# Kernel tuning notes

Hardware: AMD Instinct MI355X
Metric: run time of the kernel (lower is better)

The kernel has to match this reference:

```python
import jax, jax.numpy as jnp
import numpy as np

N_NODES = 100000
N_EDGES = 1600000
N_GRAPHS = 256
D = 128      # d_graph
H = 256      # hidden
VOCAB = 30000
OUT = 2


def setup_inputs() -> dict:
    key = jax.random.key(0)
    ks = jax.random.split(key, 24)
    def lin(k, fin, fout):
        s = 1.0 / np.sqrt(fin)
        kw, kb = jax.random.split(k)
        return (jax.random.uniform(kw, (fin, fout), jnp.float32, -s, s),
                jax.random.uniform(kb, (fout,), jnp.float32, -s, s))
    inp = {
        'feat': jax.random.randint(ks[0], (N_NODES,), 0, VOCAB),
        'src': jax.random.randint(ks[1], (N_EDGES,), 0, N_NODES),
        'dst': jax.random.randint(ks[2], (N_EDGES,), 0, N_NODES),
        'graph_id': jnp.sort(jax.random.randint(ks[3], (N_NODES,), 0, N_GRAPHS)),
        'emb': jax.random.normal(ks[4], (VOCAB, D), jnp.float32),
    }
    # SAGEConv layer 0/1: fc_self + fc_neigh + bias (mean aggregator)
    inp['ws0'], _ = lin(ks[5], D, D)
    inp['wn0'], inp['b0'] = lin(ks[6], D, D)
    inp['ws1'], _ = lin(ks[7], D, D)
    inp['wn1'], inp['b1'] = lin(ks[8], D, D)
    inp['e1_w'], inp['e1_b'] = lin(ks[9], D, H)
    inp['e2_w'], inp['e2_b'] = lin(ks[10], H, H)
    inp['e3_w'], inp['e3_b'] = lin(ks[11], H, H)
    inp['e4_w'], inp['e4_b'] = lin(ks[12], H, H)
    inp['pred_w'], inp['pred_b'] = lin(ks[13], H, OUT)
    return inp


def _sage_mean(h, src, dst, ws, wn, b):
    # gather src features, mean-scatter to dst (DGL SAGEConv 'mean')
    msg = jnp.take(h, src, axis=0)                       # [E, D]
    agg = jax.ops.segment_sum(msg, dst, num_segments=N_NODES)
    deg = jax.ops.segment_sum(jnp.ones((src.shape[0],), h.dtype), dst,
                              num_segments=N_NODES)
    h_neigh = agg / jnp.maximum(deg, 1.0)[:, None]
    return h @ ws + h_neigh @ wn + b


def reference(feat, src, dst, graph_id, emb,
              ws0, wn0, b0, ws1, wn1, b1,
              e1_w, e1_b, e2_w, e2_b, e3_w, e3_b, e4_w, e4_b,
              pred_w, pred_b):
    h = jnp.take(emb, feat, axis=0)                      # [N, D]
    h = jax.nn.relu(_sage_mean(h, src, dst, ws0, wn0, b0))
    h = jax.nn.relu(_sage_mean(h, src, dst, ws1, wn1, b1))
    # dgl.mean_nodes: per-graph mean pool
    gsum = jax.ops.segment_sum(h, graph_id, num_segments=N_GRAPHS)
    gcnt = jax.ops.segment_sum(jnp.ones((N_NODES,), h.dtype), graph_id,
                               num_segments=N_GRAPHS)
    hg = gsum / jnp.maximum(gcnt, 1.0)[:, None]          # [B, D]
    hidden = jax.nn.relu(hg @ e1_w + e1_b)
    h2 = jax.nn.relu(hidden @ e2_w + e2_b)
    h3 = jax.nn.relu(h2 @ e3_w + e3_b)
    h4 = jax.nn.relu(h3 @ e4_w + e4_b)
    y = h4 @ pred_w + pred_b
    return jax.nn.log_softmax(y, axis=1), hidden
```

## Files before the change

kernel.cpp:

```cpp
#include <hip/hip_runtime.h>
#include <hip/hip_bf16.h>
#include <math.h>

#define DF 128
#define HID 256
#define NG 256
#define CSR_CAP 768

typedef __attribute__((ext_vector_type(8))) short s8v;
typedef __attribute__((ext_vector_type(4))) float f32x4;
typedef __attribute__((ext_vector_type(2))) float f32x2;

__device__ __forceinline__ unsigned pack2bf(float lo, float hi){
  unsigned a = __bfloat16_as_ushort(__float2bfloat16(lo));
  unsigned b = __bfloat16_as_ushort(__float2bfloat16(hi));
  return a | (b<<16);
}

__global__ __launch_bounds__(256)
void k_pre0(const float* __restrict__ emb, unsigned* __restrict__ emb_f8, int nvoc,
            const int* __restrict__ dst, int* __restrict__ gb,
            const int* __restrict__ gid, float* __restrict__ gcnt,
            const float* __restrict__ ws0, const float* __restrict__ wn0,
            const float* __restrict__ ws1, const float* __restrict__ wn1,
            unsigned short* __restrict__ wt,
            int N, int E, int NC){
  __shared__ int hist[256];
  const int b = blockIdx.x, t = threadIdx.x;
  if (b < NC){
    int idx = b*256 + t;
    int total = nvoc*(DF/8);
    if (idx<total){
      const float4* e4 = (const float4*)emb;
      float4 v0 = e4[(size_t)idx*2], v1 = e4[(size_t)idx*2+1];
      unsigned w0 = __builtin_amdgcn_cvt_pk_fp8_f32(v0.x, v0.y, 0, false);
      w0 = __builtin_amdgcn_cvt_pk_fp8_f32(v0.z, v0.w, w0, true);
      unsigned w1 = __builtin_amdgcn_cvt_pk_fp8_f32(v1.x, v1.y, 0, false);
      w1 = __builtin_amdgcn_cvt_pk_fp8_f32(v1.z, v1.w, w1, true);
      ((uint2*)emb_f8)[idx] = make_uint2(w0,w1);
    }
  } else if (b < NC+256){
    int bb = b - NC;
    hist[t]=0; __syncthreads();
    for (int i = bb*256+t; i < E; i += 256*256)
      atomicAdd(&hist[dst[i]>>9], 1);
    __syncthreads();
    if (hist[t]) atomicAdd(&gb[t], hist[t]);
  } else if (b < NC+512){
    int bb = b - (NC+256);
    hist[t]=0; __syncthreads();
    for (int i = bb*256+t; i < N; i += 256*256)
      atomicAdd(&hist[gid[i]], 1);
    __syncthreads();
    if (hist[t]) atomicAdd(&gcnt[t], (float)hist[t]);
  } else {
    int bb = b - (NC+512);
    int n = bb & 127;
    int layer = bb >> 7;
    const float* ws = layer? ws1 : ws0;
    const float* wn = layer? wn1 : wn0;
    float v = (t<128)? ws[t*DF+n] : wn[(t-128)*DF+n];
    wt[((size_t)layer*DF + n)*256 + t] = __bfloat16_as_ushort(__float2bfloat16(v));
  }
}

__global__ __launch_bounds__(256)
void k_mid(const int* __restrict__ feat, const unsigned* __restrict__ emb_f8,
           unsigned* __restrict__ h_f8, int N,
           const int* __restrict__ src, const int* __restrict__ dst,
           const int* __restrict__ gb, int* __restrict__ bcur,
           unsigned* __restrict__ pairs, int E){
  const int b = blockIdx.x, t = threadIdx.x;
  if (b >= 256){
    int idx = (b-256)*256 + t;
    int total = N*8;
    if (idx<total){
      int i = idx>>3, c = idx&7;
      ((uint4*)h_f8)[idx] = ((const uint4*)emb_f8)[(size_t)feat[i]*8 + c];
    }
    return;
  }
  __shared__ int sgb[256];
  __shared__ int hist[256];
  __shared__ int base[256];
  __shared__ int cur[256];
  const int CH = (E + 255)/256;
  const int s = b*CH;
  int e = s+CH; if (e>E) e=E;
  if (s>=E) return;
  int v = gb[t];
  sgb[t]=v;
  hist[t]=0;
  __syncthreads();
  for (int o=1;o<256;o<<=1){
    int x = (t>=o)? sgb[t-o] : 0;
    __syncthreads();
    sgb[t]+=x;
    __syncthreads();
  }
  int bstart = sgb[t]-v;
  for (int i=s+t; i<e; i+=256) atomicAdd(&hist[dst[i]>>9],1);
  __syncthreads();
  if (hist[t]){ base[t] = bstart + atomicAdd(&bcur[t],hist[t]); }
  cur[t]=0;
  __syncthreads();
  for (int i=s+t; i<e; i+=256){
    int d = dst[i];
    int bk = d>>9;
    int r = atomicAdd(&cur[bk],1);
    pairs[base[bk]+r] = ((unsigned)src[i]<<9) | (unsigned)(d & 511);
  }
}

__global__ __launch_bounds__(256)
void k_bcsr(const unsigned* __restrict__ pairs, const int* __restrict__ gb,
            int* __restrict__ offs, int* __restrict__ csr, int N, int E){
  __shared__ int sgb[256];
  __shared__ int ncnt[512];
  __shared__ int noff[512];
  __shared__ int sh[256];
  const int t = threadIdx.x;
  const int b = blockIdx.x;
  const int nb0 = b<<9;
  int v = gb[t];
  sgb[t]=v;
  ncnt[t]=0; ncnt[t+256]=0;
  __syncthreads();
  for (int o=1;o<256;o<<=1){
    int x = (t>=o)? sgb[t-o] : 0;
    __syncthreads();
    sgb[t]+=x;
    __syncthreads();
  }
  const int s = sgb[b]-gb[b];
  const int e = sgb[b];
  for (int i=s+t; i<e; i+=256) atomicAdd(&ncnt[pairs[i] & 511u], 1);
  __syncthreads();
  int v0 = ncnt[2*t], v1 = ncnt[2*t+1];
  int vv = v0+v1;
  sh[t]=vv; __syncthreads();
  for (int o=1;o<256;o<<=1){
    int x=(t>=o)?sh[t-o]:0;
    __syncthreads();
    sh[t]+=x;
    __syncthreads();
  }
  int ex = sh[t]-vv;
  noff[2*t]=ex; noff[2*t+1]=ex+v0;
  __syncthreads();
  {
    int n0 = nb0 + t;
    if (n0 < N) offs[n0] = s + noff[t];
    int n1 = nb0 + t + 256;
    if (n1 < N) offs[n1] = s + noff[t+256];
    if (b == gridDim.x-1 && t==0) offs[N] = E;
  }
  ncnt[t]=0; ncnt[t+256]=0;
  __syncthreads();
  for (int i=s+t; i<e; i+=256){
    unsigned p = pairs[i];
    int d = p & 511u;
    int r = atomicAdd(&ncnt[d],1);
    csr[s + noff[d] + r] = (int)(p >> 9);
  }
}

template<int MODE>
__global__ __launch_bounds__(256,8)
void k_sage(const unsigned char* __restrict__ h_in_f8,
            const int* __restrict__ offs, const int* __restrict__ csr,
            const unsigned short* __restrict__ wt,
            const float* __restrict__ bias,
            unsigned char* __restrict__ h_out_f8,
            const int* __restrict__ gid, float* __restrict__ gsum, int N){
  __shared__ __align__(16) unsigned short s_ab[32*256];
  __shared__ int s_csr[CSR_CAP];
  __shared__ int s_gid[32];
  __shared__ float s_tmp[DF];
  const int t = threadIdx.x;
  const int node0 = blockIdx.x*32;
  const uint4* f8r = (const uint4*)h_in_f8;

  if (MODE==1 && t<32) s_gid[t] = (node0+t<N)? gid[node0+t] : -1;

  const int eBase = offs[node0];
  const int eTop  = offs[min(node0+32, N)];
  const int ecount = eTop - eBase;
  const bool useLds = (ecount <= CSR_CAP);
  if (useLds){
    for (int i=t; i<ecount; i+=256) s_csr[i] = csr[eBase+i];
  }

  const int nn = t>>3, c = t&7;
  const int sw = (nn&7)<<4;

  {
    int node = node0+nn;
    uint4 q = make_uint4(0,0,0,0);
    if (node<N) q = f8r[(size_t)node*8 + c];
    f32x2 u; unsigned pk[8];
    u=__builtin_amdgcn_cvt_pk_f32_fp8(q.x,false); pk[0]=pack2bf(u[0],u[1]);
    u=__builtin_amdgcn_cvt_pk_f32_fp8(q.x,true ); pk[1]=pack2bf(u[0],u[1]);
    u=__builtin_amdgcn_cvt_pk_f32_fp8(q.y,false); pk[2]=pack2bf(u[0],u[1]);
    u=__builtin_amdgcn_cvt_pk_f32_fp8(q.y,true ); pk[3]=pack2bf(u[0],u[1]);
    u=__builtin_amdgcn_cvt_pk_f32_fp8(q.z,false); pk[4]=pack2bf(u[0],u[1]);
    u=__builtin_amdgcn_cvt_pk_f32_fp8(q.z,true ); pk[5]=pack2bf(u[0],u[1]);
    u=__builtin_amdgcn_cvt_pk_f32_fp8(q.w,false); pk[6]=pack2bf(u[0],u[1]);
    u=__builtin_amdgcn_cvt_pk_f32_fp8(q.w,true ); pk[7]=pack2bf(u[0],u[1]);
    int byte0 = nn*512 + c*32;
    *(uint4*)((char*)s_ab + ((byte0   )^sw)) = make_uint4(pk[0],pk[1],pk[2],pk[3]);
    *(uint4*)((char*)s_ab + ((byte0+16)^sw)) = make_uint4(pk[4],pk[5],pk[6],pk[7]);
  }
  __syncthreads();

  {
    const int node = node0+nn;
    float a[16];
    #pragma unroll
    for (int j=0;j<16;j++) a[j]=0.f;
    if (node<N){
      int e0=offs[node], e1=offs[node+1];
      int deg = e1-e0;
      if (deg>0){
        #define ACC16(q) { \
          f32x2 u; \
          u=__builtin_amdgcn_cvt_pk_f32_fp8((q).x,false); a[0]+=u[0]; a[1]+=u[1]; \
          u=__builtin_amdgcn_cvt_pk_f32_fp8((q).x,true ); a[2]+=u[0]; a[3]+=u[1]; \
          u=__builtin_amdgcn_cvt_pk_f32_fp8((q).y,false); a[4]+=u[0]; a[5]+=u[1]; \
          u=__builtin_amdgcn_cvt_pk_f32_fp8((q).y,true ); a[6]+=u[0]; a[7]+=u[1]; \
          u=__builtin_amdgcn_cvt_pk_f32_fp8((q).z,false); a[8]+=u[0]; a[9]+=u[1]; \
          u=__builtin_amdgcn_cvt_pk_f32_fp8((q).z,true ); a[10]+=u[0]; a[11]+=u[1]; \
          u=__builtin_amdgcn_cvt_pk_f32_fp8((q).w,false); a[12]+=u[0]; a[13]+=u[1]; \
          u=__builtin_amdgcn_cvt_pk_f32_fp8((q).w,true ); a[14]+=u[0]; a[15]+=u[1]; }
        if (useLds){
          int le = e0 - eBase, le1 = e1 - eBase;
          for (; le+2<=le1; le+=2){
            int s0 = s_csr[le], s1 = s_csr[le+1];
            uint4 q0 = f8r[(size_t)s0*8 + c];
            uint4 q1 = f8r[(size_t)s1*8 + c];
            ACC16(q0); ACC16(q1);
          }
          if (le<le1){
            uint4 q0 = f8r[(size_t)s_csr[le]*8 + c];
            ACC16(q0);
          }
        } else {
          int e = e0;
          for (; e+2<=e1; e+=2){
            int s0 = csr[e], s1 = csr[e+1];
            uint4 q0 = f8r[(size_t)s0*8 + c];
            uint4 q1 = f8r[(size_t)s1*8 + c];
            ACC16(q0); ACC16(q1);
          }
          if (e<e1){
            uint4 q0 = f8r[(size_t)csr[e]*8 + c];
            ACC16(q0);
          }
        }
        #undef ACC16
        float inv = 1.0f/(float)deg;
        #pragma unroll
        for (int j=0;j<16;j++) a[j]*=inv;
      }
    }
    unsigned pk[8];
    #pragma unroll
    for (int j=0;j<8;j++) pk[j] = pack2bf(a[2*j],a[2*j+1]);
    int byte0 = nn*512 + 256 + c*32;
    *(uint4*)((char*)s_ab + ((byte0   )^sw)) = make_uint4(pk[0],pk[1],pk[2],pk[3]);
    *(uint4*)((char*)s_ab + ((byte0+16)^sw)) = make_uint4(pk[4],pk[5],pk[6],pk[7]);
  }

  const int wv = t>>6;
  const int lr = t&15;
  const int kg = (t&63)>>4;
  __syncthreads();

  f32x4 acc00={0,0,0,0}, acc01={0,0,0,0}, acc10={0,0,0,0}, acc11={0,0,0,0};
  const s8v* wt8 = (const s8v*)wt;
  #pragma unroll
  for (int kh=0; kh<2; kh++){
    s8v bfrag[2][4];
    #pragma unroll
    for (int ks=0; ks<4; ks++){
      int kb = (kh*4+ks)*4 + kg;
      bfrag[0][ks] = wt8[(size_t)(wv*32     + lr)*32 + kb];
      bfrag[1][ks] = wt8[(size_t)(wv*32 + 16+ lr)*32 + kb];
    }
    #pragma unroll
    for (int ks=0; ks<4; ks++){
      int cb = (kh*4+ks)*64 + kg*16;
      int r0 = lr, r1 = 16+lr;
      s8v a0 = *(const s8v*)((const char*)s_ab + ((r0*512+cb) ^ ((r0&7)<<4)));
      s8v a1 = *(const s8v*)((const char*)s_ab + ((r1*512+cb) ^ ((r1&7)<<4)));
      acc00 = __builtin_amdgcn_mfma_f32_16x16x32_bf16(a0, bfrag[0][ks], acc00, 0,0,0);
      acc01 = __builtin_amdgcn_mfma_f32_16x16x32_bf16(a0, bfrag[1][ks], acc01, 0,0,0);
      acc10 = __builtin_amdgcn_mfma_f32_16x16x32_bf16(a1, bfrag[0][ks], acc10, 0,0,0);
      acc11 = __builtin_amdgcn_mfma_f32_16x16x32_bf16(a1, bfrag[1][ks], acc11, 0,0,0);
    }
  }
  __syncthreads();

  float* cbuf = (float*)s_ab;
  #pragma unroll
  for (int r=0;r<4;r++){
    int row0 = kg*4 + r;
    cbuf[(row0   )*DF + wv*32      + lr] = acc00[r];
    cbuf[(row0   )*DF + wv*32 + 16 + lr] = acc01[r];
    cbuf[(row0+16)*DF + wv*32      + lr] = acc10[r];
    cbuf[(row0+16)*DF + wv*32 + 16 + lr] = acc11[r];
  }
  __syncthreads();

  if (MODE==0){
    int row = t>>3, c0 = (t&7)*16;
    int node = node0+row;
    if (node<N){
      float x[16];
      #pragma unroll
      for (int j=0;j<16;j++) x[j] = fmaxf(cbuf[row*DF + c0 + j] + bias[c0+j], 0.f);
      unsigned f0 = __builtin_amdgcn_cvt_pk_fp8_f32(x[0], x[1], 0, false);
      f0 = __builtin_amdgcn_cvt_pk_fp8_f32(x[2], x[3], f0, true);
      unsigned f1 = __builtin_amdgcn_cvt_pk_fp8_f32(x[4], x[5], 0, false);
      f1 = __builtin_amdgcn_cvt_pk_fp8_f32(x[6], x[7], f1, true);
      unsigned f2 = __builtin_amdgcn_cvt_pk_fp8_f32(x[8], x[9], 0, false);
      f2 = __builtin_amdgcn_cvt_pk_fp8_f32(x[10], x[11], f2, true);
      unsigned f3 = __builtin_amdgcn_cvt_pk_fp8_f32(x[12], x[13], 0, false);
      f3 = __builtin_amdgcn_cvt_pk_fp8_f32(x[14], x[15], f3, true);
      *(uint4*)&h_out_f8[(size_t)node*DF + c0] = make_uint4(f0,f1,f2,f3);
    }
  } else {
    const int d = t&127, rh = t>>7;
    const float bd = bias[d];
    int segStart = 0;
    while (segStart < 32 && s_gid[segStart] >= 0){
      int g = s_gid[segStart];
      int segEnd = segStart+1;
      while (segEnd < 32 && s_gid[segEnd] == g) segEnd++;
      float p = 0.f;
      for (int r = segStart+rh; r < segEnd; r += 2)
        p += fmaxf(cbuf[r*DF + d] + bd, 0.f);
      if (rh==1) s_tmp[d] = p;
      __syncthreads();
      if (rh==0) atomicAdd(&gsum[g*DF+d], p + s_tmp[d]);
      __syncthreads();
      segStart = segEnd;
    }
  }
}

__global__ __launch_bounds__(256)
void k_head(const float* __restrict__ gsum, const float* __restrict__ gcnt,
            const float* __restrict__ e1w, const float* __restrict__ e1b,
            const float* __restrict__ e2w, const float* __restrict__ e2b,
            const float* __restrict__ e3w, const float* __restrict__ e3b,
            const float* __restrict__ e4w, const float* __restrict__ e4b,
            const float* __restrict__ pw,  const float* __restrict__ pb,
            float* __restrict__ out, float* __restrict__ hidden){
  __shared__ float hg[DF];
  __shared__ float bufA[HID];
  __shared__ float bufB[HID];
  __shared__ float r0[HID], r1[HID];
  const int g = blockIdx.x, t = threadIdx.x;
  if (t<DF) hg[t] = gsum[g*DF+t] / fmaxf(gcnt[g],1.0f);
  __syncthreads();

  float acc = e1b[t];
  for (int k=0;k<DF;++k) acc += hg[k]*e1w[k*HID+t];
  float h1 = fmaxf(acc,0.f);
  hidden[g*HID+t] = h1;
  bufA[t] = h1;
  __syncthreads();

  acc = e2b[t];
  for (int k=0;k<HID;++k) acc += bufA[k]*e2w[k*HID+t];
  bufB[t] = fmaxf(acc,0.f);
  __syncthreads();

  acc = e3b[t];
  for (int k=0;k<HID;++k) acc += bufB[k]*e3w[k*HID+t];
  bufA[t] = fmaxf(acc,0.f);
  __syncthreads();

  acc = e4b[t];
  for (int k=0;k<HID;++k) acc += bufA[k]*e4w[k*HID+t];
  float h4 = fmaxf(acc,0.f);

  r0[t] = h4*pw[t*2+0];
  r1[t] = h4*pw[t*2+1];
  __syncthreads();
  for (int o=128;o>0;o>>=1){
    if (t<o){ r0[t]+=r0[t+o]; r1[t]+=r1[t+o]; }
    __syncthreads();
  }
  if (t==0){
    float y0 = r0[0]+pb[0], y1 = r1[0]+pb[1];
    float m = fmaxf(y0,y1);
    float l = m + logf(expf(y0-m)+expf(y1-m));
    out[g*2+0]=y0-l;
    out[g*2+1]=y1-l;
  }
}

extern "C" void kernel_launch(void* const* d_in, const int* in_sizes, int n_in,
                              void* d_out, int out_size, void* d_ws, size_t ws_size,
                              hipStream_t stream){
  const int* feat = (const int*)d_in[0];
  const int* src  = (const int*)d_in[1];
  const int* dst  = (const int*)d_in[2];
  const int* gid  = (const int*)d_in[3];
  const float* emb = (const float*)d_in[4];
  const float* ws0 = (const float*)d_in[5];
  const float* wn0 = (const float*)d_in[6];
  const float* b0  = (const float*)d_in[7];
  const float* ws1 = (const float*)d_in[8];
  const float* wn1 = (const float*)d_in[9];
  const float* b1  = (const float*)d_in[10];
  const float* e1w = (const float*)d_in[11];
  const float* e1b = (const float*)d_in[12];
  const float* e2w = (const float*)d_in[13];
  const float* e2b = (const float*)d_in[14];
  const float* e3w = (const float*)d_in[15];
  const float* e3b = (const float*)d_in[16];
  const float* e4w = (const float*)d_in[17];
  const float* e4b = (const float*)d_in[18];
  const float* pw  = (const float*)d_in[19];
  const float* pb  = (const float*)d_in[20];
  const int N = in_sizes[0];
  const int E = in_sizes[1];
  const int nvoc = in_sizes[4] / DF;

  char* basep = (char*)d_ws;
  size_t off=0;
  auto alloc=[&](size_t bytes)->void*{
    void* p = basep+off; off=(off+bytes+255)&~(size_t)255; return p;
  };
  unsigned char*  hA_f8 = (unsigned char*) alloc((size_t)N*DF);
  unsigned char*  hB_f8 = (unsigned char*) alloc((size_t)N*DF);
  unsigned char*  emb_f8= (unsigned char*) alloc((size_t)nvoc*DF);
  int*   offs  = (int*)  alloc((size_t)(N+1)*4);
  int*   csr   = (int*)  alloc((size_t)E*4);
  int*   gb    = (int*)  alloc(1024);
  int*   bcur  = (int*)  alloc(1024);
  unsigned short* wtb = (unsigned short*)alloc((size_t)2*DF*256*2);
  float* gsum  = (float*)alloc((size_t)NG*DF*4);
  float* gcnt  = (float*)alloc((size_t)NG*4);
  unsigned* pairs = (unsigned*)alloc((size_t)E*4);
  float* out    = (float*)d_out;
  float* hidden = out + NG*2;

  hipMemsetAsync(gb, 0, 1024, stream);
  hipMemsetAsync(bcur, 0, 1024, stream);
  hipMemsetAsync(gsum, 0, (size_t)NG*DF*4, stream);
  hipMemsetAsync(gcnt, 0, (size_t)NG*4, stream);

  const int NBK = (N+511)>>9;
  const int NC = (nvoc*(DF/8) + 255)/256;
  const int NP1 = (N*8 + 255)/256;
  k_pre0<<<NC+768,256,0,stream>>>(emb,(unsigned*)emb_f8,nvoc,
                                  dst,gb,gid,gcnt,
                                  ws0,wn0,ws1,wn1,wtb,N,E,NC);
  k_mid<<<256+NP1,256,0,stream>>>(feat,(const unsigned*)emb_f8,
                                  (unsigned*)hA_f8,N,
                                  src,dst,gb,bcur,pairs,E);
  k_bcsr<<<NBK,256,0,stream>>>(pairs,gb,offs,csr,N,E);

  k_sage<0><<<(N+31)/32,256,0,stream>>>(hA_f8,offs,csr,wtb,        b0,
                                        hB_f8,nullptr,nullptr,N);
  k_sage<1><<<(N+31)/32,256,0,stream>>>(hB_f8,offs,csr,wtb+DF*256, b1,
                                        nullptr,gid,gsum,N);

  k_head<<<NG,HID,0,stream>>>(gsum,gcnt,e1w,e1b,e2w,e2b,e3w,e3b,e4w,e4b,
                              pw,pb,out,hidden);
}
```

Before: 207.2 us.

## Bucket edges into 8 coarse mega-buckets, then filter per fine bucket in CSR build

The first scatter pass now groups edges into 8 mega-buckets of 16384 destination nodes instead of 256 buckets of 512 nodes. Each pair packs src<<14 with the low 14 bits of dst. The second pass still uses one block per 512-node bucket, but each block scans its whole mega-bucket and keeps only matching entries. The aim is fewer, more contiguous scatter targets and fewer global atomics in the first pass. In exchange, the CSR pass reads each pair about 32 times, and shared-memory atomics in the first pass now pile up on just 8 counters.

Result: slower. 782.3 us (+277.5%).

```diff
diff --git a/kernel.cpp b/kernel.cpp
--- a/kernel.cpp
+++ b/kernel.cpp
@@ -68,8 +68,8 @@
 void k_mid(const int* __restrict__ feat, const unsigned* __restrict__ emb_f8,
            unsigned* __restrict__ h_f8, int N,
            const int* __restrict__ src, const int* __restrict__ dst,
-           const int* __restrict__ gb, int* __restrict__ bcur,
-           unsigned* __restrict__ pairs, int E){
+           const int* __restrict__ gb, int* __restrict__ mbcur,
+           unsigned* __restrict__ pairs1, int E){
   const int b = blockIdx.x, t = threadIdx.x;
   if (b >= 256){
     int idx = (b-256)*256 + t;
@@ -81,16 +81,17 @@
     return;
   }
   __shared__ int sgb[256];
-  __shared__ int hist[256];
-  __shared__ int base[256];
-  __shared__ int cur[256];
+  __shared__ int mstart[8];
+  __shared__ int hist1[8];
+  __shared__ int base1[8];
+  __shared__ int cur1[8];
   const int CH = (E + 255)/256;
   const int s = b*CH;
   int e = s+CH; if (e>E) e=E;
   if (s>=E) return;
   int v = gb[t];
   sgb[t]=v;
-  hist[t]=0;
+  if (t<8){ hist1[t]=0; cur1[t]=0; }
   __syncthreads();
   for (int o=1;o<256;o<<=1){
     int x = (t>=o)? sgb[t-o] : 0;
@@ -98,30 +99,32 @@
     sgb[t]+=x;
     __syncthreads();
   }
-  int bstart = sgb[t]-v;
-  for (int i=s+t; i<e; i+=256) atomicAdd(&hist[dst[i]>>9],1);
-  __syncthreads();
-  if (hist[t]){ base[t] = bstart + atomicAdd(&bcur[t],hist[t]); }
-  cur[t]=0;
+  if ((t&31)==0) mstart[t>>5] = sgb[t]-v;
+  __syncthreads();
+  for (int i=s+t; i<e; i+=256) atomicAdd(&hist1[dst[i]>>14],1);
+  __syncthreads();
+  if (t<8 && hist1[t]) base1[t] = mstart[t] + atomicAdd(&mbcur[t],hist1[t]);
   __syncthreads();
   for (int i=s+t; i<e; i+=256){
     int d = dst[i];
-    int bk = d>>9;
-    int r = atomicAdd(&cur[bk],1);
-    pairs[base[bk]+r] = ((unsigned)src[i]<<9) | (unsigned)(d & 511);
+    int m = d>>14;
+    int r = atomicAdd(&cur1[m],1);
+    pairs1[base1[m]+r] = ((unsigned)src[i]<<14) | (unsigned)(d & 16383);
   }
 }
 
 __global__ __launch_bounds__(256)
-void k_bcsr(const unsigned* __restrict__ pairs, const int* __restrict__ gb,
-            int* __restrict__ offs, int* __restrict__ csr, int N, int E){
+void k_bcsr2(const unsigned* __restrict__ pairs1, const int* __restrict__ gb,
+             int* __restrict__ offs, int* __restrict__ csr, int N, int E, int NBK){
   __shared__ int sgb[256];
   __shared__ int ncnt[512];
   __shared__ int noff[512];
   __shared__ int sh[256];
   const int t = threadIdx.x;
-  const int b = blockIdx.x;
-  const int nb0 = b<<9;
+  const int fb = blockIdx.x;
+  const int m  = fb >> 5;
+  const int lf = fb & 31;
+  const int nb0 = fb << 9;
   int v = gb[t];
   sgb[t]=v;
   ncnt[t]=0; ncnt[t+256]=0;
@@ -132,9 +135,13 @@
     sgb[t]+=x;
     __syncthreads();
   }
-  const int s = sgb[b]-gb[b];
-  const int e = sgb[b];
-  for (int i=s+t; i<e; i+=256) atomicAdd(&ncnt[pairs[i] & 511u], 1);
+  const int fstart = sgb[fb] - gb[fb];
+  const int ms = sgb[m*32] - gb[m*32];
+  const int me = sgb[m*32+31];
+  for (int i=ms+t; i<me; i+=256){
+    unsigned d14 = pairs1[i] & 16383u;
+    if ((int)(d14>>9) == lf) atomicAdd(&ncnt[d14 & 511u], 1);
+  }
   __syncthreads();
   int v0 = ncnt[2*t], v1 = ncnt[2*t+1];
   int vv = v0+v1;
@@ -150,18 +157,21 @@
   __syncthreads();
   {
     int n0 = nb0 + t;
-    if (n0 < N) offs[n0] = s + noff[t];
+    if (n0 < N) offs[n0] = fstart + noff[t];
     int n1 = nb0 + t + 256;
-    if (n1 < N) offs[n1] = s + noff[t+256];
-    if (b == gridDim.x-1 && t==0) offs[N] = E;
+    if (n1 < N) offs[n1] = fstart + noff[t+256];
+    if (fb == NBK-1 && t==0) offs[N] = E;
   }
   ncnt[t]=0; ncnt[t+256]=0;
   __syncthreads();
-  for (int i=s+t; i<e; i+=256){
-    unsigned p = pairs[i];
-    int d = p & 511u;
-    int r = atomicAdd(&ncnt[d],1);
-    csr[s + noff[d] + r] = (int)(p >> 9);
+  for (int i=ms+t; i<me; i+=256){
+    unsigned p = pairs1[i];
+    unsigned d14 = p & 16383u;
+    if ((int)(d14>>9) == lf){
+      int d = d14 & 511u;
+      int r = atomicAdd(&ncnt[d],1);
+      csr[fstart + noff[d] + r] = (int)(p >> 14);
+    }
   }
 }
 
@@ -441,16 +451,16 @@
   int*   offs  = (int*)  alloc((size_t)(N+1)*4);
   int*   csr   = (int*)  alloc((size_t)E*4);
   int*   gb    = (int*)  alloc(1024);
-  int*   bcur  = (int*)  alloc(1024);
+  int*   mbcur = (int*)  alloc(1024);
   unsigned short* wtb = (unsigned short*)alloc((size_t)2*DF*256*2);
   float* gsum  = (float*)alloc((size_t)NG*DF*4);
   float* gcnt  = (float*)alloc((size_t)NG*4);
-  unsigned* pairs = (unsigned*)alloc((size_t)E*4);
+  unsigned* pairs1 = (unsigned*)alloc((size_t)E*4);
   float* out    = (float*)d_out;
   float* hidden = out + NG*2;
 
   hipMemsetAsync(gb, 0, 1024, stream);
-  hipMemsetAsync(bcur, 0, 1024, stream);
+  hipMemsetAsync(mbcur, 0, 1024, stream);
   hipMemsetAsync(gsum, 0, (size_t)NG*DF*4, stream);
   hipMemsetAsync(gcnt, 0, (size_t)NG*4, stream);
 
@@ -462,8 +472,8 @@
                                   ws0,wn0,ws1,wn1,wtb,N,E,NC);
   k_mid<<<256+NP1,256,0,stream>>>(feat,(const unsigned*)emb_f8,
                                   (unsigned*)hA_f8,N,
-                                  src,dst,gb,bcur,pairs,E);
-  k_bcsr<<<NBK,256,0,stream>>>(pairs,gb,offs,csr,N,E);
+                                  src,dst,gb,mbcur,pairs1,E);
+  k_bcsr2<<<NBK,256,0,stream>>>(pairs1,gb,offs,csr,N,E,NBK);
 
   k_sage<0><<<(N+31)/32,256,0,stream>>>(hA_f8,offs,csr,wtb,        b0,
                                         hB_f8,nullptr,nullptr,N);
```

## Stage edge binning in shared memory for coalesced bucket writes

Applied to the files above, without the earlier changes.

The edge-binning kernel now handles fixed chunks of 6144 edges per block. It sorts each chunk locally by bucket in LDS, using a block-wide prefix scan over the bucket histogram, and then writes the pairs out as contiguous runs per bucket. Before, each edge was scattered straight to global memory. The aim is better coalesced stores, at the cost of roughly 37KB of LDS per block, an extra scan, and a different block count (about 261 instead of 256).

Result: no change. 207.1 us (-0.0%).

```diff
diff --git a/kernel.cpp b/kernel.cpp
--- a/kernel.cpp
+++ b/kernel.cpp
@@ -6,6 +6,7 @@
 #define HID 256
 #define NG 256
 #define CSR_CAP 768
+#define BINB 6144
 
 typedef __attribute__((ext_vector_type(8))) short s8v;
 typedef __attribute__((ext_vector_type(4))) float f32x4;
@@ -69,10 +70,10 @@
            unsigned* __restrict__ h_f8, int N,
            const int* __restrict__ src, const int* __restrict__ dst,
            const int* __restrict__ gb, int* __restrict__ bcur,
-           unsigned* __restrict__ pairs, int E){
+           unsigned* __restrict__ pairs, int E, int NBB){
   const int b = blockIdx.x, t = threadIdx.x;
-  if (b >= 256){
-    int idx = (b-256)*256 + t;
+  if (b >= NBB){
+    int idx = (b-NBB)*256 + t;
     int total = N*8;
     if (idx<total){
       int i = idx>>3, c = idx&7;
@@ -82,15 +83,18 @@
   }
   __shared__ int sgb[256];
   __shared__ int hist[256];
-  __shared__ int base[256];
+  __shared__ int choff[256];
   __shared__ int cur[256];
-  const int CH = (E + 255)/256;
-  const int s = b*CH;
-  int e = s+CH; if (e>E) e=E;
+  __shared__ int gbase[256];
+  __shared__ unsigned stag[BINB];
+  __shared__ unsigned short sbkt[BINB];
+  const int s = b*BINB;
+  int e = s+BINB; if (e>E) e=E;
   if (s>=E) return;
+  const int len = e - s;
+
   int v = gb[t];
-  sgb[t]=v;
-  hist[t]=0;
+  sgb[t]=v; hist[t]=0; cur[t]=0;
   __syncthreads();
   for (int o=1;o<256;o<<=1){
     int x = (t>=o)? sgb[t-o] : 0;
@@ -98,17 +102,36 @@
     sgb[t]+=x;
     __syncthreads();
   }
-  int bstart = sgb[t]-v;
+  const int bstart = sgb[t]-v;
+
   for (int i=s+t; i<e; i+=256) atomicAdd(&hist[dst[i]>>9],1);
   __syncthreads();
-  if (hist[t]){ base[t] = bstart + atomicAdd(&bcur[t],hist[t]); }
-  cur[t]=0;
+  {
+    int hv = hist[t];
+    choff[t]=hv; __syncthreads();
+    for (int o=1;o<256;o<<=1){
+      int x = (t>=o)? choff[t-o] : 0;
+      __syncthreads();
+      choff[t]+=x;
+      __syncthreads();
+    }
+    int ex = choff[t]-hv;
+    __syncthreads();
+    choff[t]=ex;
+    if (hv) gbase[t] = bstart + atomicAdd(&bcur[t], hv);
+  }
   __syncthreads();
   for (int i=s+t; i<e; i+=256){
     int d = dst[i];
     int bk = d>>9;
-    int r = atomicAdd(&cur[bk],1);
-    pairs[base[bk]+r] = ((unsigned)src[i]<<9) | (unsigned)(d & 511);
+    int r = choff[bk] + atomicAdd(&cur[bk],1);
+    stag[r] = ((unsigned)src[i]<<9) | (unsigned)(d & 511);
+    sbkt[r] = (unsigned short)bk;
+  }
+  __syncthreads();
+  for (int i=t; i<len; i+=256){
+    int bk = sbkt[i];
+    pairs[gbase[bk] + (i - choff[bk])] = stag[i];
   }
 }
 
@@ -457,12 +480,13 @@
   const int NBK = (N+511)>>9;
   const int NC = (nvoc*(DF/8) + 255)/256;
   const int NP1 = (N*8 + 255)/256;
+  const int NBB = (E + BINB-1)/BINB;
   k_pre0<<<NC+768,256,0,stream>>>(emb,(unsigned*)emb_f8,nvoc,
                                   dst,gb,gid,gcnt,
                                   ws0,wn0,ws1,wn1,wtb,N,E,NC);
-  k_mid<<<256+NP1,256,0,stream>>>(feat,(const unsigned*)emb_f8,
+  k_mid<<<NBB+NP1,256,0,stream>>>(feat,(const unsigned*)emb_f8,
                                   (unsigned*)hA_f8,N,
-                                  src,dst,gb,bcur,pairs,E);
+                                  src,dst,gb,bcur,pairs,E,NBB);
   k_bcsr<<<NBK,256,0,stream>>>(pairs,gb,offs,csr,N,E);
 
   k_sage<0><<<(N+31)/32,256,0,stream>>>(hA_f8,offs,csr,wtb,        b0,
```
